# Kernel optimization log

Measured on AMD Instinct MI355X. Metric: run time of the kernel, lower is better.

The kernel has to match this reference:

```python
import jax, jax.numpy as jnp
import numpy as np

SCALE = 128.0  # init arg; divisor is sqrt(scale)
NEG_BIG = -1e10

def setup_inputs() -> dict:
    key = jax.random.key(0)
    kq, kk, kv, km = jax.random.split(key, 4)
    B, Nq, Nk, D = 16, 2048, 2048, 128
    q = jax.random.normal(kq, (B, Nq, D), dtype=jnp.float32)
    k = jax.random.normal(kk, (B, Nk, D), dtype=jnp.float32)
    v = jax.random.normal(kv, (B, Nk, D), dtype=jnp.float32)
    mask = jax.random.randint(km, (B, Nq, Nk), 0, 2).astype(bool)
    return {"q": q, "k": k, "v": v, "mask": mask}

def reference(q, k, v, mask):
    inv = 1.0 / np.sqrt(SCALE).astype(np.float32)
    # scores: [b, q, k]
    scores = jnp.einsum('bqd,bkd->bqk', q, k) * inv
    scores = jnp.where(mask, NEG_BIG, scores)
    att = jax.nn.softmax(scores, axis=-1)
    context = jnp.einsum('bqk,bkd->bqd', att, v)
    return (context, att)
```

## Files before the change

kernel.cpp:

```cpp
#include <hip/hip_runtime.h>

#define B_ 16
#define NQ 2048
#define NK 2048
#define DH 128
#define INV 0.08838834764831843f

typedef __attribute__((ext_vector_type(8))) short bf16x8;
typedef __attribute__((ext_vector_type(4))) float f32x4;

typedef const __attribute__((address_space(1))) unsigned int* gas1_t;
typedef __attribute__((address_space(3))) unsigned int* las3_t;

__device__ __forceinline__ unsigned short f2b(float f) {
  unsigned u = __float_as_uint(f);
  u += 0x7fff + ((u >> 16) & 1);
  return (unsigned short)(u >> 16);
}

__device__ __forceinline__ void gl_lds16(const unsigned short* g, unsigned short* l) {
  __builtin_amdgcn_global_load_lds((gas1_t)g, (las3_t)l, 16, 0, 0);
}

__global__ __launch_bounds__(256) void k_cvt(
    const float* __restrict__ src, unsigned short* __restrict__ dst, int n4) {
  int i = blockIdx.x * 256 + threadIdx.x;
  if (i >= n4) return;
  float4 f = ((const float4*)src)[i];
  ushort4 u;
  u.x = f2b(f.x); u.y = f2b(f.y); u.z = f2b(f.z); u.w = f2b(f.w);
  ((ushort4*)dst)[i] = u;
}

__global__ __launch_bounds__(256) void k_trans(
    const float* __restrict__ v, unsigned short* __restrict__ vt) {
  __shared__ float tile[32][33];
  const int b = blockIdx.z, kv0 = blockIdx.x << 5, d0 = blockIdx.y << 5;
  const int tx = threadIdx.x & 31, ty = threadIdx.x >> 5;
  #pragma unroll
  for (int i = 0; i < 4; i++)
    tile[ty + 8*i][tx] = v[((size_t)b*NK + kv0 + ty + 8*i)*DH + d0 + tx];
  __syncthreads();
  #pragma unroll
  for (int i = 0; i < 4; i++)
    vt[((size_t)b*DH + d0 + ty + 8*i)*NK + kv0 + tx] = f2b(tile[tx][ty + 8*i]);
}

__global__ __launch_bounds__(256, 4) void k_attn(
    const unsigned short* __restrict__ qb, const unsigned short* __restrict__ kb,
    const unsigned short* __restrict__ vtb, const int* __restrict__ mask,
    float* __restrict__ att, float* __restrict__ ctx) {
  __shared__ unsigned short KA[64*128];
  __shared__ unsigned short VA[128*64];
  __shared__ unsigned short Ps[32*64];
  __shared__ float Lrow[32];

  const int t = threadIdx.x;
  const int wave = t >> 6, lane = t & 63, quad = lane >> 4, l15 = lane & 15;
  const int rh = wave >> 1, nh = wave & 1;

  const int p = blockIdx.x + (blockIdx.y << 6);
  const int lid = ((p & 7) << 7) + (p >> 3);
  const int b = lid >> 6, q0 = (lid & 63) << 5;

  const unsigned short* qg = qb  + ((size_t)b*NQ + q0)*DH;
  const unsigned short* kg = kb  + (size_t)b*NK*DH;
  const unsigned short* vg = vtb + (size_t)b*DH*NK;
  const int* mg   = mask + ((size_t)b*NQ + q0)*NK;
  float*     attg = att  + ((size_t)b*NQ + q0)*NK;
  float*     cg   = ctx  + ((size_t)b*NQ + q0)*DH;

  if (t < 32) Lrow[t] = 0.f;

  bf16x8 qf[4];
  { const unsigned short* qr = qg + (size_t)(rh*16 + l15)*DH + quad*8;
    #pragma unroll
    for (int kd = 0; kd < 4; kd++) qf[kd] = *(const bf16x8*)(qr + kd*32); }

  const int row0 = rh*16 + quad*4;
  const int* mgR[4]; float* attR[4];
  #pragma unroll
  for (int r = 0; r < 4; r++) {
    mgR[r]  = mg   + (size_t)(row0 + r)*NK + nh*32 + l15;
    attR[r] = attg + (size_t)(row0 + r)*NK + nh*32 + l15;
  }

  const int kr0 = nh*32 + l15, kr1 = kr0 + 16;
  const int kbs0 = (kr0 << 8) ^ ((kr0 & 7) << 4);
  const int kbs1 = (kr1 << 8) ^ ((kr1 & 7) << 4);
  const int pr  = rh*16 + l15;
  const int pbs = (pr << 7) ^ ((pr & 7) << 4);
  int vbs[4];
  #pragma unroll
  for (int dt = 0; dt < 4; dt++) {
    int d = nh*64 + dt*16 + l15;
    vbs[dt] = (d << 7) ^ ((d & 7) << 4);
  }

  auto stageK = [&](unsigned short* buf, const unsigned short* src) {
    #pragma unroll
    for (int i = 0; i < 4; i++) {
      int L = (wave << 12) + (i << 10) + (lane << 4);
      int row = L >> 8;
      int cb  = (L & 255) ^ ((row & 7) << 4);
      gl_lds16(src + ((size_t)row << 7) + (cb >> 1), buf + (L >> 1));
    }
  };
  auto stageV = [&](const unsigned short* src) {
    #pragma unroll
    for (int i = 0; i < 4; i++) {
      int L = (wave << 12) + (i << 10) + (lane << 4);
      int d  = L >> 7;
      int cb = (L & 127) ^ ((d & 7) << 4);
      gl_lds16(src + (size_t)d*NK + (cb >> 1), VA + (L >> 1));
    }
  };
  auto loadMask = [&](int k0, int* mr) {
    #pragma unroll
    for (int nt = 0; nt < 2; nt++)
      #pragma unroll
      for (int r = 0; r < 4; r++)
        mr[nt*4 + r] = __builtin_nontemporal_load(mgR[r] + k0 + nt*16);
  };
  auto qkt = [&](const unsigned short* buf, f32x4& s0v, f32x4& s1v) {
    s0v = 0; s1v = 0;
    const char* bc = (const char*)buf;
    __builtin_amdgcn_s_setprio(1);
    #pragma unroll
    for (int kd = 0; kd < 4; kd++) {
      int cb = (kd*32 + quad*8) << 1;
      bf16x8 b0 = *(const bf16x8*)(bc + (kbs0 ^ cb));
      bf16x8 b1 = *(const bf16x8*)(bc + (kbs1 ^ cb));
      s0v = __builtin_amdgcn_mfma_f32_16x16x32_bf16(qf[kd], b0, s0v, 0, 0, 0);
      s1v = __builtin_amdgcn_mfma_f32_16x16x32_bf16(qf[kd], b1, s1v, 0, 0, 0);
    }
    __builtin_amdgcn_s_setprio(0);
  };

  unsigned mw0=0,mw1=0,mw2=0,mw3=0,mw4=0,mw5=0,mw6=0,mw7=0;
  float ls[4] = {0.f, 0.f, 0.f, 0.f};

  auto epi1 = [&](const int* mr, const f32x4& s0v, const f32x4& s1v) {
    unsigned nb = 0;
    #pragma unroll
    for (int nt = 0; nt < 2; nt++) {
      const f32x4& sv = nt ? s1v : s0v;
      #pragma unroll
      for (int r = 0; r < 4; r++) {
        float e = __expf(sv[r]*INV);
        if (mr[nt*4 + r] != 0) { nb |= 1u << (nt*4 + r); e = 0.f; }
        ls[r] += e;
      }
    }
    mw0=(mw0>>8)|(mw1<<24); mw1=(mw1>>8)|(mw2<<24); mw2=(mw2>>8)|(mw3<<24);
    mw3=(mw3>>8)|(mw4<<24); mw4=(mw4>>8)|(mw5<<24); mw5=(mw5>>8)|(mw6<<24);
    mw6=(mw6>>8)|(mw7<<24); mw7=(mw7>>8)|(nb<<24);
  };

  int mrA[8], mrB[8];
  stageK(KA, kg);
  loadMask(0, mrA);

  for (int t2 = 0; t2 < 32; t2 += 2) {
    __builtin_amdgcn_s_barrier();
    asm volatile("" ::: "memory");
    stageK(VA, kg + (size_t)(t2+1)*64*DH);
    loadMask((t2+1)*64, mrB);
    asm volatile("s_waitcnt vmcnt(12)" ::: "memory");
    __builtin_amdgcn_s_barrier();
    asm volatile("" ::: "memory");
    { f32x4 s0, s1; qkt(KA, s0, s1); epi1(mrA, s0, s1); }

    __builtin_amdgcn_s_barrier();
    asm volatile("" ::: "memory");
    if (t2 + 2 < 32) {
      stageK(KA, kg + (size_t)(t2+2)*64*DH);
      loadMask((t2+2)*64, mrA);
      asm volatile("s_waitcnt vmcnt(12)" ::: "memory");
    } else {
      asm volatile("s_waitcnt vmcnt(0)" ::: "memory");
    }
    __builtin_amdgcn_s_barrier();
    asm volatile("" ::: "memory");
    { f32x4 s0, s1; qkt(VA, s0, s1); epi1(mrB, s0, s1); }
  }

  __syncthreads();
  #pragma unroll
  for (int r = 0; r < 4; r++) atomicAdd(&Lrow[row0 + r], ls[r]);
  __syncthreads();
  float il[4];
  #pragma unroll
  for (int r = 0; r < 4; r++) il[r] = 1.0f / Lrow[row0 + r];

  f32x4 ca[4];
  #pragma unroll
  for (int dt = 0; dt < 4; dt++) ca[dt] = 0;

  stageK(KA, kg);
  for (int tt = 0; tt < 32; tt++) {
    __builtin_amdgcn_s_barrier();
    asm volatile("" ::: "memory");
    stageV(vg + tt*64);
    asm volatile("s_waitcnt vmcnt(4)" ::: "memory");
    __builtin_amdgcn_s_barrier();
    asm volatile("" ::: "memory");
    f32x4 s0, s1;
    qkt(KA, s0, s1);

    unsigned nb = mw0 & 255u;
    mw0=(mw0>>8)|(mw1<<24); mw1=(mw1>>8)|(mw2<<24); mw2=(mw2>>8)|(mw3<<24);
    mw3=(mw3>>8)|(mw4<<24); mw4=(mw4>>8)|(mw5<<24); mw5=(mw5>>8)|(mw6<<24);
    mw6=(mw6>>8)|(mw7<<24); mw7>>=8;
    #pragma unroll
    for (int nt = 0; nt < 2; nt++) {
      const f32x4& sv = nt ? s1 : s0;
      #pragma unroll
      for (int r = 0; r < 4; r++) {
        float e = __expf(sv[r]*INV) * il[r];
        if ((nb >> (nt*4 + r)) & 1) e = 0.f;
        __builtin_nontemporal_store(e, attR[r] + tt*64 + nt*16);
        int row = row0 + r;
        int cbw = ((nh*32 + nt*16 + l15) << 1) ^ ((row & 7) << 4);
        *(unsigned short*)((char*)Ps + (row << 7) + cbw) = f2b(e);
      }
    }
    asm volatile("s_waitcnt vmcnt(8) lgkmcnt(0)" ::: "memory");
    __builtin_amdgcn_s_barrier();
    asm volatile("" ::: "memory");
    if (tt + 1 < 32) stageK(KA, kg + (size_t)(tt+1)*64*DH);

    __builtin_amdgcn_s_setprio(1);
    #pragma unroll
    for (int kv = 0; kv < 2; kv++) {
      int cb = (kv*32 + quad*8) << 1;
      bf16x8 pa = *(const bf16x8*)((const char*)Ps + (pbs ^ cb));
      #pragma unroll
      for (int dt = 0; dt < 4; dt++) {
        bf16x8 vb = *(const bf16x8*)((const char*)VA + (vbs[dt] ^ cb));
        ca[dt] = __builtin_amdgcn_mfma_f32_16x16x32_bf16(pa, vb, ca[dt], 0, 0, 0);
      }
    }
    __builtin_amdgcn_s_setprio(0);
  }

  #pragma unroll
  for (int dt = 0; dt < 4; dt++)
    #pragma unroll
    for (int r = 0; r < 4; r++)
      cg[(size_t)(row0 + r)*DH + nh*64 + dt*16 + l15] = ca[dt][r];
}

extern "C" void kernel_launch(void* const* d_in, const int* in_sizes, int n_in,
                              void* d_out, int out_size, void* d_ws, size_t ws_size,
                              hipStream_t stream) {
  const float* q = (const float*)d_in[0];
  const float* k = (const float*)d_in[1];
  const float* v = (const float*)d_in[2];
  const int* mask = (const int*)d_in[3];
  float* ctx = (float*)d_out;
  float* att = ctx + (size_t)B_*NQ*DH;

  const size_t NE = (size_t)B_*NQ*DH;
  unsigned short* qws = (unsigned short*)d_ws;
  unsigned short* kws = qws + NE;
  unsigned short* vws = kws + NE;

  k_cvt  <<<(int)(NE/1024), 256, 0, stream>>>(q, qws, (int)(NE/4));
  k_cvt  <<<(int)(NE/1024), 256, 0, stream>>>(k, kws, (int)(NE/4));
  k_trans<<<dim3(NK/32, DH/32, B_), 256, 0, stream>>>(v, vws);
  k_attn <<<dim3(NQ/32, B_), 256, 0, stream>>>(qws, kws, vws, mask, att, ctx);
}
```

Baseline: 572.5 us.

## Load K and V fragments directly from global into registers, double-buffer K in LDS

In the first pass, K fragments are read straight from global memory into registers and the LDS staging and barriers are dropped. In the second pass, V fragments are loaded directly into registers, and K is double-buffered in LDS (KA/KB) with staging of the next tile issued at the top of each iteration. The att store is changed from a nontemporal store to a normal store. The aim is to remove LDS traffic and barrier stalls, at the cost of uncoalesced global loads per lane and more register pressure.

Measured after the change: 705.9 us. +23.3%, slower.

```diff
diff --git a/kernel.cpp b/kernel.cpp
--- a/kernel.cpp
+++ b/kernel.cpp
@@ -51,7 +51,7 @@
     const unsigned short* __restrict__ vtb, const int* __restrict__ mask,
     float* __restrict__ att, float* __restrict__ ctx) {
   __shared__ unsigned short KA[64*128];
-  __shared__ unsigned short VA[128*64];
+  __shared__ unsigned short KB[64*128];
   __shared__ unsigned short Ps[32*64];
   __shared__ float Lrow[32];
 
@@ -90,12 +90,6 @@
   const int kbs1 = (kr1 << 8) ^ ((kr1 & 7) << 4);
   const int pr  = rh*16 + l15;
   const int pbs = (pr << 7) ^ ((pr & 7) << 4);
-  int vbs[4];
-  #pragma unroll
-  for (int dt = 0; dt < 4; dt++) {
-    int d = nh*64 + dt*16 + l15;
-    vbs[dt] = (d << 7) ^ ((d & 7) << 4);
-  }
 
   auto stageK = [&](unsigned short* buf, const unsigned short* src) {
     #pragma unroll
@@ -104,15 +98,6 @@
       int row = L >> 8;
       int cb  = (L & 255) ^ ((row & 7) << 4);
       gl_lds16(src + ((size_t)row << 7) + (cb >> 1), buf + (L >> 1));
-    }
-  };
-  auto stageV = [&](const unsigned short* src) {
-    #pragma unroll
-    for (int i = 0; i < 4; i++) {
-      int L = (wave << 12) + (i << 10) + (lane << 4);
-      int d  = L >> 7;
-      int cb = (L & 127) ^ ((d & 7) << 4);
-      gl_lds16(src + (size_t)d*NK + (cb >> 1), VA + (L >> 1));
     }
   };
   auto loadMask = [&](int k0, int* mr) {
@@ -136,6 +121,26 @@
     }
     __builtin_amdgcn_s_setprio(0);
   };
+  const unsigned short* kR0 = kg + (size_t)kr0*DH + quad*8;
+  const unsigned short* kR1 = kg + (size_t)kr1*DH + quad*8;
+  auto qkt_dir = [&](int k0, f32x4& s0v, f32x4& s1v) {
+    const unsigned short* a0 = kR0 + (size_t)k0*DH;
+    const unsigned short* a1 = kR1 + (size_t)k0*DH;
+    bf16x8 b0[4], b1[4];
+    #pragma unroll
+    for (int kd = 0; kd < 4; kd++) {
+      b0[kd] = *(const bf16x8*)(a0 + kd*32);
+      b1[kd] = *(const bf16x8*)(a1 + kd*32);
+    }
+    s0v = 0; s1v = 0;
+    __builtin_amdgcn_s_setprio(1);
+    #pragma unroll
+    for (int kd = 0; kd < 4; kd++) {
+      s0v = __builtin_amdgcn_mfma_f32_16x16x32_bf16(qf[kd], b0[kd], s0v, 0, 0, 0);
+      s1v = __builtin_amdgcn_mfma_f32_16x16x32_bf16(qf[kd], b1[kd], s1v, 0, 0, 0);
+    }
+    __builtin_amdgcn_s_setprio(0);
+  };
 
   unsigned mw0=0,mw1=0,mw2=0,mw3=0,mw4=0,mw5=0,mw6=0,mw7=0;
   float ls[4] = {0.f, 0.f, 0.f, 0.f};
@@ -157,37 +162,21 @@
     mw6=(mw6>>8)|(mw7<<24); mw7=(mw7>>8)|(nb<<24);
   };
 
+  stageK(KA, kg);
+
   int mrA[8], mrB[8];
-  stageK(KA, kg);
   loadMask(0, mrA);
-
   for (int t2 = 0; t2 < 32; t2 += 2) {
-    __builtin_amdgcn_s_barrier();
-    asm volatile("" ::: "memory");
-    stageK(VA, kg + (size_t)(t2+1)*64*DH);
     loadMask((t2+1)*64, mrB);
-    asm volatile("s_waitcnt vmcnt(12)" ::: "memory");
-    __builtin_amdgcn_s_barrier();
-    asm volatile("" ::: "memory");
-    { f32x4 s0, s1; qkt(KA, s0, s1); epi1(mrA, s0, s1); }
-
-    __builtin_amdgcn_s_barrier();
-    asm volatile("" ::: "memory");
-    if (t2 + 2 < 32) {
-      stageK(KA, kg + (size_t)(t2+2)*64*DH);
-      loadMask((t2+2)*64, mrA);
-      asm volatile("s_waitcnt vmcnt(12)" ::: "memory");
-    } else {
-      asm volatile("s_waitcnt vmcnt(0)" ::: "memory");
-    }
-    __builtin_amdgcn_s_barrier();
-    asm volatile("" ::: "memory");
-    { f32x4 s0, s1; qkt(VA, s0, s1); epi1(mrB, s0, s1); }
+    { f32x4 s0, s1; qkt_dir(t2*64, s0, s1); epi1(mrA, s0, s1); }
+    if (t2 + 2 < 32) loadMask((t2+2)*64, mrA);
+    { f32x4 s0, s1; qkt_dir((t2+1)*64, s0, s1); epi1(mrB, s0, s1); }
   }
 
   __syncthreads();
   #pragma unroll
   for (int r = 0; r < 4; r++) atomicAdd(&Lrow[row0 + r], ls[r]);
+  asm volatile("s_waitcnt vmcnt(0)" ::: "memory");
   __syncthreads();
   float il[4];
   #pragma unroll
@@ -197,16 +186,27 @@
   #pragma unroll
   for (int dt = 0; dt < 4; dt++) ca[dt] = 0;
 
-  stageK(KA, kg);
+  const unsigned short* vR[4];
+  #pragma unroll
+  for (int dt = 0; dt < 4; dt++)
+    vR[dt] = vg + (size_t)(nh*64 + dt*16 + l15)*NK + quad*8;
+
   for (int tt = 0; tt < 32; tt++) {
-    __builtin_amdgcn_s_barrier();
-    asm volatile("" ::: "memory");
-    stageV(vg + tt*64);
-    asm volatile("s_waitcnt vmcnt(4)" ::: "memory");
-    __builtin_amdgcn_s_barrier();
-    asm volatile("" ::: "memory");
+    const unsigned short* cur = (tt & 1) ? KB : KA;
+    unsigned short* nxt = (tt & 1) ? KA : KB;
+
+    if (tt + 1 < 32) stageK(nxt, kg + (size_t)(tt+1)*64*DH);
+    __builtin_amdgcn_sched_barrier(0);
+    bf16x8 vf0[4], vf1[4];
+    #pragma unroll
+    for (int dt = 0; dt < 4; dt++) {
+      vf0[dt] = *(const bf16x8*)(vR[dt] + tt*64);
+      vf1[dt] = *(const bf16x8*)(vR[dt] + tt*64 + 32);
+    }
+    __builtin_amdgcn_sched_barrier(0);
+
     f32x4 s0, s1;
-    qkt(KA, s0, s1);
+    qkt(cur, s0, s1);
 
     unsigned nb = mw0 & 255u;
     mw0=(mw0>>8)|(mw1<<24); mw1=(mw1>>8)|(mw2<<24); mw2=(mw2>>8)|(mw3<<24);
@@ -219,16 +219,16 @@
       for (int r = 0; r < 4; r++) {
         float e = __expf(sv[r]*INV) * il[r];
         if ((nb >> (nt*4 + r)) & 1) e = 0.f;
-        __builtin_nontemporal_store(e, attR[r] + tt*64 + nt*16);
+        attR[r][tt*64 + nt*16] = e;
         int row = row0 + r;
         int cbw = ((nh*32 + nt*16 + l15) << 1) ^ ((row & 7) << 4);
         *(unsigned short*)((char*)Ps + (row << 7) + cbw) = f2b(e);
       }
     }
-    asm volatile("s_waitcnt vmcnt(8) lgkmcnt(0)" ::: "memory");
+    asm volatile("s_waitcnt lgkmcnt(0)" ::: "memory");
     __builtin_amdgcn_s_barrier();
     asm volatile("" ::: "memory");
-    if (tt + 1 < 32) stageK(KA, kg + (size_t)(tt+1)*64*DH);
+    asm volatile("s_waitcnt vmcnt(8)" ::: "memory");
 
     __builtin_amdgcn_s_setprio(1);
     #pragma unroll
@@ -237,11 +237,17 @@
       bf16x8 pa = *(const bf16x8*)((const char*)Ps + (pbs ^ cb));
       #pragma unroll
       for (int dt = 0; dt < 4; dt++) {
-        bf16x8 vb = *(const bf16x8*)((const char*)VA + (vbs[dt] ^ cb));
+        const bf16x8 vb = kv ? vf1[dt] : vf0[dt];
         ca[dt] = __builtin_amdgcn_mfma_f32_16x16x32_bf16(pa, vb, ca[dt], 0, 0, 0);
       }
     }
     __builtin_amdgcn_s_setprio(0);
+
+    if (tt + 1 < 32) {
+      asm volatile("s_waitcnt vmcnt(16) lgkmcnt(0)" ::: "memory");
+      __builtin_amdgcn_s_barrier();
+      asm volatile("" ::: "memory");
+    }
   }
 
   #pragma unroll
```
